# Performance work log

Hardware: AMD Instinct MI355X
Metric: run time of the kernel (lower is better)

## Reference

```python
import jax, jax.numpy as jnp
import numpy as np

N_NODES = 50000
N_EDGES = 640000
D_IN = 128
D_OUT = 128


def setup_inputs() -> dict:
    key = jax.random.key(0)
    k1, k2, k3, k4 = jax.random.split(key, 4)
    x = jax.random.normal(k1, (N_NODES, D_IN), dtype=jnp.float32)
    edge_index = jax.random.randint(k2, (2, N_EDGES), 0, N_NODES, dtype=jnp.int64)
    weight = jax.random.uniform(k3, (1,), dtype=jnp.float32)
    temperature = jnp.ones((1,), dtype=jnp.float32)
    W = jax.random.normal(k4, (D_IN, D_OUT), dtype=jnp.float32) * (1.0 / np.sqrt(D_IN))
    b = jnp.zeros((D_OUT,), dtype=jnp.float32)
    return {"x": x, "edge_index": edge_index, "weight": weight,
            "temperature": temperature, "W": W, "b": b}


def _gcn_conv(x, edge_index, W, b):
    N = x.shape[0]
    src, dst = edge_index[0], edge_index[1]
    loop = jnp.arange(N, dtype=edge_index.dtype)
    s = jnp.concatenate([src, loop])  # self-loops appended
    d = jnp.concatenate([dst, loop])
    deg = jax.ops.segment_sum(jnp.ones(s.shape[0], dtype=x.dtype), d, num_segments=N)
    dinv = jnp.where(deg > 0, deg ** -0.5, 0.0)
    norm = dinv[s] * dinv[d]  # [E+N]
    h = x @ W                 # linear transform first (PyG GCNConv)
    msg = h[s] * norm[:, None]
    out = jax.ops.segment_sum(msg, d, num_segments=N)
    return out + b


def _gradient_entropy(x, edge_index, temperature):
    # Boltzmann distribution over per-node Dirichlet energies;
    # entropy gradient w.r.t. node features (computed with autodiff).
    N = x.shape[0]
    src, dst = edge_index[0], edge_index[1]

    def entropy(z):
        diff = z[src] - z[dst]                                  # [E, D]
        E = jax.ops.segment_sum(jnp.sum(diff * diff, axis=-1), dst, num_segments=N)
        logp = jax.nn.log_softmax(-E / temperature[0])
        p = jnp.exp(logp)
        return -jnp.sum(p * logp)

    return jax.grad(entropy)(x)


def reference(x, edge_index, weight, temperature, W, b):
    h = _gcn_conv(x, edge_index, W, b)
    g = jax.lax.stop_gradient(_gradient_entropy(h, edge_index, temperature))
    return h + weight * g
```

## Files before the change

kernel.cpp:

```cpp
#include <hip/hip_runtime.h>

#define N_NODES 50000
#define N_EDGES 640000
#define NSCANB  196
#define MAXD    64
#define NBUCK   196
#define BUCKCAP 4096
#define EPB     2048
#define NPARTB  313

#define OFF_HTMPB    0
#define OFF_OBF      3200000
#define OFF_DEG      6400000
#define OFF_DINV     6450000
#define OFF_E        6500000
#define OFF_PMIN     6550000
#define OFF_PS0      6550256
#define OFF_PS1      6550512
#define OFF_WT       6550768
#define OFF_GCUR     6558960
#define OFF_PART     6559216
#define OFF_EBIN     7362032

typedef __attribute__((ext_vector_type(8))) short bf16x8;
typedef __attribute__((ext_vector_type(4))) float f32x4;

__device__ __forceinline__ unsigned short f2bf(float f) {
    unsigned u = __float_as_uint(f);
    unsigned r = u + 0x7fffu + ((u >> 16) & 1u);
    return (unsigned short)(r >> 16);
}
__device__ __forceinline__ float bflo(unsigned u) { return __uint_as_float(u << 16); }
__device__ __forceinline__ float bfhi(unsigned u) { return __uint_as_float(u & 0xffff0000u); }

__global__ __launch_bounds__(256) void k_init(const float* __restrict__ W,
                                              int* __restrict__ gcursor,
                                              unsigned short* __restrict__ wtg) {
    int gtid = blockIdx.x * 256 + threadIdx.x;
    if (gtid < NBUCK) gcursor[gtid] = 0;
    if (gtid < 4096) {
        int k = gtid >> 5, n4 = (gtid & 31) * 4;
        float4 v = *(const float4*)(W + k * 128 + n4);
        wtg[(n4 + 0) * 128 + k] = f2bf(v.x);
        wtg[(n4 + 1) * 128 + k] = f2bf(v.y);
        wtg[(n4 + 2) * 128 + k] = f2bf(v.z);
        wtg[(n4 + 3) * 128 + k] = f2bf(v.w);
    }
}

__global__ __launch_bounds__(256) void k_part(const int* __restrict__ src,
                                              const int* __restrict__ dst,
                                              int* __restrict__ gcursor,
                                              unsigned* __restrict__ part) {
    __shared__ int hist[NBUCK];
    __shared__ int base[NBUCK];
    int tid = threadIdx.x;
    if (tid < NBUCK) hist[tid] = 0;
    __syncthreads();
    int e0 = blockIdx.x * EPB;
    unsigned val[8]; int bk[8]; int rk[8];
    #pragma unroll
    for (int j = 0; j < 8; j++) {
        int e = e0 + j * 256 + tid;
        if (e < N_EDGES) {
            int s = src[e], d = dst[e];
            int bc = d >> 8;
            if ((unsigned)bc >= NBUCK) bc = NBUCK - 1;
            bk[j] = bc;
            val[j] = ((unsigned)(d & 255) << 16) | ((unsigned)s & 0xffffu);
            rk[j] = atomicAdd(&hist[bc], 1);
        } else { bk[j] = -1; val[j] = 0u; rk[j] = 0; }
    }
    __syncthreads();
    if (tid < NBUCK) base[tid] = atomicAdd(&gcursor[tid], hist[tid]);
    __syncthreads();
    #pragma unroll
    for (int j = 0; j < 8; j++) {
        if (bk[j] >= 0) {
            int p = base[bk[j]] + rk[j];
            if ((unsigned)p < BUCKCAP) part[bk[j] * BUCKCAP + p] = val[j];
        }
    }
}

__global__ __launch_bounds__(256) void k_bin(const int* __restrict__ gcursor,
                                             const unsigned* __restrict__ part,
                                             unsigned short* __restrict__ ebin,
                                             int* __restrict__ deg,
                                             float* __restrict__ dinv) {
    __shared__ __align__(16) unsigned short bins[256][MAXD];
    __shared__ int cnt[256];
    int tid = threadIdx.x, bkt = blockIdx.x;
    cnt[tid] = 0;
    __syncthreads();
    int M = gcursor[bkt];
    if (M > BUCKCAP) M = BUCKCAP;
    if (M < 0) M = 0;
    for (int i = tid; i < M; i += 256) {
        unsigned v = part[bkt * BUCKCAP + i];
        int ln = (v >> 16) & 255;
        int pos = atomicAdd(&cnt[ln], 1);
        if (pos < MAXD) bins[ln][pos] = (unsigned short)(v & 0xffffu);
    }
    __syncthreads();
    int node = bkt * 256 + tid;
    if (node < N_NODES) {
        int dg = cnt[tid]; if (dg > MAXD) dg = MAXD;
        deg[node] = dg;
        dinv[node] = rsqrtf((float)(dg + 1));
    }
    int nvalid = N_NODES - bkt * 256; if (nvalid > 256) nvalid = 256;
    if (nvalid < 0) nvalid = 0;
    int lim = nvalid * MAXD / 8;
    const uint4* bs = (const uint4*)&bins[0][0];
    uint4* gb = (uint4*)(ebin + (size_t)bkt * 256 * MAXD);
    for (int i = tid; i < lim; i += 256) gb[i] = bs[i];
}

__global__ __launch_bounds__(256) void k_gemm(const float* __restrict__ x,
                                              const unsigned short* __restrict__ wtg,
                                              const float* __restrict__ dinv,
                                              unsigned short* __restrict__ htmpb) {
    int tid = threadIdx.x;
    int wave = tid >> 6, lane = tid & 63, quad = lane >> 4, m16 = lane & 15;
    int r0 = blockIdx.x * 32 + (wave & 1) * 16;
    int ch = (wave >> 1) * 4;
    int arow = r0 + m16;
    int rowc = arow < N_NODES ? arow : N_NODES - 1;
    f32x4 acc[4];
    #pragma unroll
    for (int c = 0; c < 4; c++) acc[c] = (f32x4){0.f, 0.f, 0.f, 0.f};
    #pragma unroll
    for (int kt = 0; kt < 4; kt++) {
        int koff = kt * 32 + quad * 8;
        float4 xa = *(const float4*)(x + rowc * 128 + koff);
        float4 xb = *(const float4*)(x + rowc * 128 + koff + 4);
        bf16x8 af;
        af[0] = (short)f2bf(xa.x); af[1] = (short)f2bf(xa.y);
        af[2] = (short)f2bf(xa.z); af[3] = (short)f2bf(xa.w);
        af[4] = (short)f2bf(xb.x); af[5] = (short)f2bf(xb.y);
        af[6] = (short)f2bf(xb.z); af[7] = (short)f2bf(xb.w);
        #pragma unroll
        for (int c = 0; c < 4; c++) {
            bf16x8 bfrag = *(const bf16x8*)(wtg + ((ch + c) * 16 + m16) * 128 + koff);
            acc[c] = __builtin_amdgcn_mfma_f32_16x16x32_bf16(af, bfrag, acc[c], 0, 0, 0);
        }
    }
    #pragma unroll
    for (int reg = 0; reg < 4; reg++) {
        int grow = r0 + quad * 4 + reg;
        if (grow < N_NODES) {
            float dv = dinv[grow];
            #pragma unroll
            for (int c = 0; c < 4; c++)
                htmpb[grow * 128 + (ch + c) * 16 + m16] = f2bf(acc[c][reg] * dv);
        }
    }
}

__global__ __launch_bounds__(256) void k_gather(const unsigned short* __restrict__ htmpb,
                                                const int* __restrict__ deg,
                                                const float* __restrict__ dinv,
                                                const float* __restrict__ b,
                                                const unsigned short* __restrict__ ebin,
                                                float* __restrict__ out,
                                                unsigned short* __restrict__ obf) {
    int node = blockIdx.x * 16 + (threadIdx.x >> 4);
    int lane = threadIdx.x & 15;
    int c8 = lane * 8;
    int dg = deg[node]; if (dg > MAXD) dg = MAXD; if (dg < 0) dg = 0;
    float di = dinv[node];
    float4 bv0 = *(const float4*)(b + c8);
    float4 bv1 = *(const float4*)(b + c8 + 4);
    uint4 hv = *(const uint4*)(htmpb + node * 128 + c8);
    float a0 = bflo(hv.x), a1 = bfhi(hv.x), a2 = bflo(hv.y), a3 = bfhi(hv.y);
    float a4 = bflo(hv.z), a5 = bfhi(hv.z), a6 = bflo(hv.w), a7 = bfhi(hv.w);
    float c0 = 0.f, c1 = 0.f, c2c = 0.f, c3 = 0.f, c4 = 0.f, c5 = 0.f, c6 = 0.f, c7 = 0.f;
    const unsigned short* bin = ebin + node * MAXD;
    int k = 0;
    for (; k + 3 < dg; k += 4) {
        uint2 bw = *(const uint2*)(bin + k);
        int s0 = bw.x & 0xffff, s1 = bw.x >> 16;
        int s2 = bw.y & 0xffff, s3 = bw.y >> 16;
        uint4 u0 = *(const uint4*)(htmpb + s0 * 128 + c8);
        uint4 u1 = *(const uint4*)(htmpb + s1 * 128 + c8);
        uint4 u2 = *(const uint4*)(htmpb + s2 * 128 + c8);
        uint4 u3 = *(const uint4*)(htmpb + s3 * 128 + c8);
        a0 += bflo(u0.x); a1 += bfhi(u0.x); a2 += bflo(u0.y); a3 += bfhi(u0.y);
        a4 += bflo(u0.z); a5 += bfhi(u0.z); a6 += bflo(u0.w); a7 += bfhi(u0.w);
        c0 += bflo(u1.x); c1 += bfhi(u1.x); c2c += bflo(u1.y); c3 += bfhi(u1.y);
        c4 += bflo(u1.z); c5 += bfhi(u1.z); c6 += bflo(u1.w); c7 += bfhi(u1.w);
        a0 += bflo(u2.x); a1 += bfhi(u2.x); a2 += bflo(u2.y); a3 += bfhi(u2.y);
        a4 += bflo(u2.z); a5 += bfhi(u2.z); a6 += bflo(u2.w); a7 += bfhi(u2.w);
        c0 += bflo(u3.x); c1 += bfhi(u3.x); c2c += bflo(u3.y); c3 += bfhi(u3.y);
        c4 += bflo(u3.z); c5 += bfhi(u3.z); c6 += bflo(u3.w); c7 += bfhi(u3.w);
    }
    for (; k < dg; k++) {
        int s0 = bin[k];
        uint4 u0 = *(const uint4*)(htmpb + s0 * 128 + c8);
        a0 += bflo(u0.x); a1 += bfhi(u0.x); a2 += bflo(u0.y); a3 += bfhi(u0.y);
        a4 += bflo(u0.z); a5 += bfhi(u0.z); a6 += bflo(u0.w); a7 += bfhi(u0.w);
    }
    a0 += c0; a1 += c1; a2 += c2c; a3 += c3; a4 += c4; a5 += c5; a6 += c6; a7 += c7;
    a0 = bv0.x + di * a0; a1 = bv0.y + di * a1; a2 = bv0.z + di * a2; a3 = bv0.w + di * a3;
    a4 = bv1.x + di * a4; a5 = bv1.y + di * a5; a6 = bv1.z + di * a6; a7 = bv1.w + di * a7;
    *(float4*)(out + node * 128 + c8)     = make_float4(a0, a1, a2, a3);
    *(float4*)(out + node * 128 + c8 + 4) = make_float4(a4, a5, a6, a7);
    uint4 pk;
    pk.x = (unsigned)f2bf(a0) | ((unsigned)f2bf(a1) << 16);
    pk.y = (unsigned)f2bf(a2) | ((unsigned)f2bf(a3) << 16);
    pk.z = (unsigned)f2bf(a4) | ((unsigned)f2bf(a5) << 16);
    pk.w = (unsigned)f2bf(a6) | ((unsigned)f2bf(a7) << 16);
    *(uint4*)(obf + node * 128 + c8) = pk;
}

__global__ __launch_bounds__(256) void k_energy(const unsigned short* __restrict__ obf,
                                                const int* __restrict__ deg,
                                                const unsigned short* __restrict__ ebin,
                                                float* __restrict__ E) {
    int node = blockIdx.x * 16 + (threadIdx.x >> 4);
    int lane = threadIdx.x & 15;
    int c8 = lane * 8;
    int dg = deg[node]; if (dg > MAXD) dg = MAXD; if (dg < 0) dg = 0;
    uint4 ud = *(const uint4*)(obf + node * 128 + c8);
    float o0 = bflo(ud.x), o1 = bfhi(ud.x), o2 = bflo(ud.y), o3 = bfhi(ud.y);
    float o4 = bflo(ud.z), o5 = bfhi(ud.z), o6 = bflo(ud.w), o7 = bfhi(ud.w);
    float acc = 0.f, acc2 = 0.f;
    const unsigned short* bin = ebin + node * MAXD;
    int k = 0;
    for (; k + 3 < dg; k += 4) {
        uint2 bw = *(const uint2*)(bin + k);
        int s0 = bw.x & 0xffff, s1 = bw.x >> 16;
        int s2 = bw.y & 0xffff, s3 = bw.y >> 16;
        uint4 a = *(const uint4*)(obf + s0 * 128 + c8);
        uint4 c = *(const uint4*)(obf + s1 * 128 + c8);
        uint4 g = *(const uint4*)(obf + s2 * 128 + c8);
        uint4 h = *(const uint4*)(obf + s3 * 128 + c8);
        float d0, d1, d2, d3, d4, d5, d6, d7;
        d0 = bflo(a.x) - o0; d1 = bfhi(a.x) - o1; d2 = bflo(a.y) - o2; d3 = bfhi(a.y) - o3;
        d4 = bflo(a.z) - o4; d5 = bfhi(a.z) - o5; d6 = bflo(a.w) - o6; d7 = bfhi(a.w) - o7;
        acc  += d0*d0 + d1*d1 + d2*d2 + d3*d3 + d4*d4 + d5*d5 + d6*d6 + d7*d7;
        d0 = bflo(c.x) - o0; d1 = bfhi(c.x) - o1; d2 = bflo(c.y) - o2; d3 = bfhi(c.y) - o3;
        d4 = bflo(c.z) - o4; d5 = bfhi(c.z) - o5; d6 = bflo(c.w) - o6; d7 = bfhi(c.w) - o7;
        acc2 += d0*d0 + d1*d1 + d2*d2 + d3*d3 + d4*d4 + d5*d5 + d6*d6 + d7*d7;
        d0 = bflo(g.x) - o0; d1 = bfhi(g.x) - o1; d2 = bflo(g.y) - o2; d3 = bfhi(g.y) - o3;
        d4 = bflo(g.z) - o4; d5 = bfhi(g.z) - o5; d6 = bflo(g.w) - o6; d7 = bfhi(g.w) - o7;
        acc  += d0*d0 + d1*d1 + d2*d2 + d3*d3 + d4*d4 + d5*d5 + d6*d6 + d7*d7;
        d0 = bflo(h.x) - o0; d1 = bfhi(h.x) - o1; d2 = bflo(h.y) - o2; d3 = bfhi(h.y) - o3;
        d4 = bflo(h.z) - o4; d5 = bfhi(h.z) - o5; d6 = bflo(h.w) - o6; d7 = bfhi(h.w) - o7;
        acc2 += d0*d0 + d1*d1 + d2*d2 + d3*d3 + d4*d4 + d5*d5 + d6*d6 + d7*d7;
    }
    for (; k < dg; k++) {
        int s0 = bin[k];
        uint4 a = *(const uint4*)(obf + s0 * 128 + c8);
        float d0 = bflo(a.x) - o0, d1 = bfhi(a.x) - o1, d2 = bflo(a.y) - o2, d3 = bfhi(a.y) - o3;
        float d4 = bflo(a.z) - o4, d5 = bfhi(a.z) - o5, d6 = bflo(a.w) - o6, d7 = bfhi(a.w) - o7;
        acc += d0*d0 + d1*d1 + d2*d2 + d3*d3 + d4*d4 + d5*d5 + d6*d6 + d7*d7;
    }
    acc += acc2;
    #pragma unroll
    for (int off = 8; off; off >>= 1) acc += __shfl_xor(acc, off);
    if (lane == 0) E[node] = acc;
}

__global__ __launch_bounds__(256) void k_esoft(const float* __restrict__ E,
                                               const float* __restrict__ temp,
                                               float* __restrict__ pmin,
                                               float* __restrict__ ps0,
                                               float* __restrict__ ps1) {
    __shared__ float fred[12];
    int tid = threadIdx.x;
    int i = blockIdx.x * 256 + tid;
    int lane = tid & 63, wid = tid >> 6;
    float e = (i < N_NODES) ? E[i] : 3.402823466e38f;
    float m = e;
    #pragma unroll
    for (int off = 32; off; off >>= 1) m = fminf(m, __shfl_xor(m, off));
    if (lane == 0) fred[wid] = m;
    __syncthreads();
    float bm = fminf(fminf(fred[0], fred[1]), fminf(fred[2], fred[3]));
    float T = temp[0];
    float s0 = 0.f, s1 = 0.f;
    if (i < N_NODES) {
        float dd = (bm - e) / T;
        float ed = __expf(dd);
        s0 = ed; s1 = ed * dd;
    }
    #pragma unroll
    for (int off = 32; off; off >>= 1) { s0 += __shfl_xor(s0, off); s1 += __shfl_xor(s1, off); }
    __syncthreads();
    if (lane == 0) { fred[4 + wid] = s0; fred[8 + wid] = s1; }
    __syncthreads();
    if (tid == 0) {
        pmin[blockIdx.x] = bm;
        ps0[blockIdx.x] = fred[4] + fred[5] + fred[6] + fred[7];
        ps1[blockIdx.x] = fred[8] + fred[9] + fred[10] + fred[11];
    }
}

__global__ __launch_bounds__(256) void k_grad(const int* __restrict__ deg,
                                              const unsigned short* __restrict__ ebin,
                                              const float* __restrict__ E,
                                              const float* __restrict__ temp,
                                              const float* __restrict__ pmin,
                                              const float* __restrict__ ps0,
                                              const float* __restrict__ ps1,
                                              const float* __restrict__ weight,
                                              float* __restrict__ out) {
    __shared__ float fred[12];
    int tid = threadIdx.x;
    int lane = tid & 63, wid = tid >> 6;

    float pm = (tid < NSCANB) ? pmin[tid] : 3.402823466e38f;
    float m = pm;
    #pragma unroll
    for (int off = 32; off; off >>= 1) m = fminf(m, __shfl_xor(m, off));
    if (lane == 0) fred[wid] = m;
    __syncthreads();
    float gmin = fminf(fminf(fred[0], fred[1]), fminf(fred[2], fred[3]));
    float T = temp[0];
    float s0 = 0.f, s1 = 0.f;
    if (tid < NSCANB) {
        float dl = (gmin - pm) / T;
        float ex = __expf(dl);
        float b0 = ps0[tid], b1 = ps1[tid];
        s0 = ex * b0;
        s1 = ex * (b1 + dl * b0);
    }
    #pragma unroll
    for (int off = 32; off; off >>= 1) { s0 += __shfl_xor(s0, off); s1 += __shfl_xor(s1, off); }
    __syncthreads();
    if (lane == 0) { fred[4 + wid] = s0; fred[8 + wid] = s1; }
    __syncthreads();
    float S0 = fred[4] + fred[5] + fred[6] + fred[7];
    float S1 = fred[8] + fred[9] + fred[10] + fred[11];

    float wscale = 2.f * weight[0];
    int lane32 = tid & 31;
    int node = blockIdx.x * 8 + (tid >> 5);
    if (node >= N_NODES) return;
    float dd = (gmin - E[node]) / T;
    float qd = (__expf(dd) / S0) * (dd - S1 / S0) / T;
    if (qd == 0.f) return;
    float cc = wscale * qd;
    int dg = deg[node]; if (dg > MAXD) dg = MAXD; if (dg < 0) dg = 0;
    float4 od = *(const float4*)(out + node * 128 + lane32 * 4);
    float sx = 0.f, sy = 0.f, sz = 0.f, sw = 0.f;
    const unsigned short* bin = ebin + node * MAXD;
    for (int k = 0; k < dg; k++) {
        int s = bin[k];
        if (s >= N_NODES) s = N_NODES - 1;
        float4 a = *(const float4*)(out + s * 128 + lane32 * 4);
        float vx = cc * (a.x - od.x), vy = cc * (a.y - od.y);
        float vz = cc * (a.z - od.z), vw = cc * (a.w - od.w);
        float* os = out + s * 128 + lane32 * 4;
        atomicAdd(os + 0, vx); atomicAdd(os + 1, vy);
        atomicAdd(os + 2, vz); atomicAdd(os + 3, vw);
        sx += vx; sy += vy; sz += vz; sw += vw;
    }
    float* odp = out + node * 128 + lane32 * 4;
    atomicAdd(odp + 0, -sx); atomicAdd(odp + 1, -sy);
    atomicAdd(odp + 2, -sz); atomicAdd(odp + 3, -sw);
}

extern "C" void kernel_launch(void* const* d_in, const int* in_sizes, int n_in,
                              void* d_out, int out_size, void* d_ws, size_t ws_size,
                              hipStream_t stream) {
    const float* x      = (const float*)d_in[0];
    const int*   ei     = (const int*)d_in[1];
    const float* weight = (const float*)d_in[2];
    const float* temp   = (const float*)d_in[3];
    const float* W      = (const float*)d_in[4];
    const float* b      = (const float*)d_in[5];
    float* out = (float*)d_out;
    float* ws  = (float*)d_ws;

    const int* src = ei;
    const int* dst = ei + N_EDGES;

    unsigned short* htmpb = (unsigned short*)(ws + OFF_HTMPB);
    unsigned short* obf   = (unsigned short*)(ws + OFF_OBF);
    int*   deg      = (int*)(ws + OFF_DEG);
    float* dinv     = ws + OFF_DINV;
    float* Earr     = ws + OFF_E;
    float* pminA    = ws + OFF_PMIN;
    float* ps0A     = ws + OFF_PS0;
    float* ps1A     = ws + OFF_PS1;
    unsigned short* wtg = (unsigned short*)(ws + OFF_WT);
    int*   gcursor  = (int*)(ws + OFF_GCUR);
    unsigned* part  = (unsigned*)(ws + OFF_PART);
    unsigned short* ebin = (unsigned short*)(ws + OFF_EBIN);

    k_init<<<16, 256, 0, stream>>>(W, gcursor, wtg);
    k_part<<<NPARTB, 256, 0, stream>>>(src, dst, gcursor, part);
    k_bin<<<NBUCK, 256, 0, stream>>>(gcursor, part, ebin, deg, dinv);
    k_gemm<<<1563, 256, 0, stream>>>(x, wtg, dinv, htmpb);
    k_gather<<<3125, 256, 0, stream>>>(htmpb, deg, dinv, b, ebin, out, obf);
    k_energy<<<3125, 256, 0, stream>>>(obf, deg, ebin, Earr);
    k_esoft<<<NSCANB, 256, 0, stream>>>(Earr, temp, pminA, ps0A, ps1A);
    k_grad<<<6250, 256, 0, stream>>>(deg, ebin, Earr, temp, pminA, ps0A, ps1A, weight, out);
}
```

Measured before the change: 215.6 us.

## Process nodes in degree-sorted order in gather and energy kernels

Builds a per-degree histogram in k_bin and adds a k_order kernel that counting-sorts node ids by in-degree. The gather and energy kernels then take their node from this order array, so the 16-lane groups in a wave handle nodes of similar degree. This is meant to cut divergence and load imbalance from the variable-length neighbour loops. The cost is an extra kernel launch, global atomics, an extra indirection per node, and writes to out/obf that are no longer contiguous across groups.

```diff
diff --git a/kernel.cpp b/kernel.cpp
--- a/kernel.cpp
+++ b/kernel.cpp
@@ -21,6 +21,9 @@
 #define OFF_GCUR     6558960
 #define OFF_PART     6559216
 #define OFF_EBIN     7362032
+#define OFF_DHIST    8962032
+#define OFF_GDCUR    8962100
+#define OFF_ORDER    8962200
 
 typedef __attribute__((ext_vector_type(8))) short bf16x8;
 typedef __attribute__((ext_vector_type(4))) float f32x4;
@@ -35,9 +38,12 @@
 
 __global__ __launch_bounds__(256) void k_init(const float* __restrict__ W,
                                               int* __restrict__ gcursor,
+                                              int* __restrict__ dhist,
+                                              int* __restrict__ gdcur,
                                               unsigned short* __restrict__ wtg) {
     int gtid = blockIdx.x * 256 + threadIdx.x;
     if (gtid < NBUCK) gcursor[gtid] = 0;
+    if (gtid < 65) { dhist[gtid] = 0; gdcur[gtid] = 0; }
     if (gtid < 4096) {
         int k = gtid >> 5, n4 = (gtid & 31) * 4;
         float4 v = *(const float4*)(W + k * 128 + n4);
@@ -87,11 +93,14 @@
                                              const unsigned* __restrict__ part,
                                              unsigned short* __restrict__ ebin,
                                              int* __restrict__ deg,
-                                             float* __restrict__ dinv) {
+                                             float* __restrict__ dinv,
+                                             int* __restrict__ dhist) {
     __shared__ __align__(16) unsigned short bins[256][MAXD];
     __shared__ int cnt[256];
+    __shared__ int dh[65];
     int tid = threadIdx.x, bkt = blockIdx.x;
     cnt[tid] = 0;
+    if (tid < 65) dh[tid] = 0;
     __syncthreads();
     int M = gcursor[bkt];
     if (M > BUCKCAP) M = BUCKCAP;
@@ -108,13 +117,49 @@
         int dg = cnt[tid]; if (dg > MAXD) dg = MAXD;
         deg[node] = dg;
         dinv[node] = rsqrtf((float)(dg + 1));
-    }
+        atomicAdd(&dh[dg], 1);
+    }
+    __syncthreads();
+    if (tid < 65 && dh[tid] > 0) atomicAdd(&dhist[tid], dh[tid]);
     int nvalid = N_NODES - bkt * 256; if (nvalid > 256) nvalid = 256;
     if (nvalid < 0) nvalid = 0;
     int lim = nvalid * MAXD / 8;
     const uint4* bs = (const uint4*)&bins[0][0];
     uint4* gb = (uint4*)(ebin + (size_t)bkt * 256 * MAXD);
     for (int i = tid; i < lim; i += 256) gb[i] = bs[i];
+}
+
+__global__ __launch_bounds__(256) void k_order(const int* __restrict__ deg,
+                                               const int* __restrict__ dhist,
+                                               int* __restrict__ gdcur,
+                                               int* __restrict__ order) {
+    __shared__ int dh[65];
+    __shared__ int resv[65];
+    __shared__ int pre[65];
+    __shared__ int hval[65];
+    int tid = threadIdx.x;
+    int node = blockIdx.x * 256 + tid;
+    if (tid < 65) { dh[tid] = 0; hval[tid] = dhist[tid]; }
+    __syncthreads();
+    int dg = 0, rk = 0;
+    bool valid = node < N_NODES;
+    if (valid) {
+        dg = deg[node];
+        if (dg < 0) dg = 0; if (dg > MAXD) dg = MAXD;
+        rk = atomicAdd(&dh[dg], 1);
+    }
+    __syncthreads();
+    if (tid < 65) resv[tid] = dh[tid] > 0 ? atomicAdd(&gdcur[tid], dh[tid]) : 0;
+    if (tid == 0) {
+        int run = 0;
+        #pragma unroll 1
+        for (int d = 0; d < 65; d++) { pre[d] = run; run += hval[d]; }
+    }
+    __syncthreads();
+    if (valid) {
+        int pos = pre[dg] + resv[dg] + rk;
+        if ((unsigned)pos < N_NODES) order[pos] = node;
+    }
 }
 
 __global__ __launch_bounds__(256) void k_gemm(const float* __restrict__ x,
@@ -163,9 +208,12 @@
                                                 const float* __restrict__ dinv,
                                                 const float* __restrict__ b,
                                                 const unsigned short* __restrict__ ebin,
+                                                const int* __restrict__ order,
                                                 float* __restrict__ out,
                                                 unsigned short* __restrict__ obf) {
-    int node = blockIdx.x * 16 + (threadIdx.x >> 4);
+    int idx = blockIdx.x * 16 + (threadIdx.x >> 4);
+    int node = order[idx];
+    if ((unsigned)node >= N_NODES) node = 0;
     int lane = threadIdx.x & 15;
     int c8 = lane * 8;
     int dg = deg[node]; if (dg > MAXD) dg = MAXD; if (dg < 0) dg = 0;
@@ -217,8 +265,11 @@
 __global__ __launch_bounds__(256) void k_energy(const unsigned short* __restrict__ obf,
                                                 const int* __restrict__ deg,
                                                 const unsigned short* __restrict__ ebin,
+                                                const int* __restrict__ order,
                                                 float* __restrict__ E) {
-    int node = blockIdx.x * 16 + (threadIdx.x >> 4);
+    int idx = blockIdx.x * 16 + (threadIdx.x >> 4);
+    int node = order[idx];
+    if ((unsigned)node >= N_NODES) node = 0;
     int lane = threadIdx.x & 15;
     int c8 = lane * 8;
     int dg = deg[node]; if (dg > MAXD) dg = MAXD; if (dg < 0) dg = 0;
@@ -390,13 +441,17 @@
     int*   gcursor  = (int*)(ws + OFF_GCUR);
     unsigned* part  = (unsigned*)(ws + OFF_PART);
     unsigned short* ebin = (unsigned short*)(ws + OFF_EBIN);
-
-    k_init<<<16, 256, 0, stream>>>(W, gcursor, wtg);
+    int*   dhist    = (int*)(ws + OFF_DHIST);
+    int*   gdcur    = (int*)(ws + OFF_GDCUR);
+    int*   order    = (int*)(ws + OFF_ORDER);
+
+    k_init<<<16, 256, 0, stream>>>(W, gcursor, dhist, gdcur, wtg);
     k_part<<<NPARTB, 256, 0, stream>>>(src, dst, gcursor, part);
-    k_bin<<<NBUCK, 256, 0, stream>>>(gcursor, part, ebin, deg, dinv);
+    k_bin<<<NBUCK, 256, 0, stream>>>(gcursor, part, ebin, deg, dinv, dhist);
+    k_order<<<NSCANB, 256, 0, stream>>>(deg, dhist, gdcur, order);
     k_gemm<<<1563, 256, 0, stream>>>(x, wtg, dinv, htmpb);
-    k_gather<<<3125, 256, 0, stream>>>(htmpb, deg, dinv, b, ebin, out, obf);
-    k_energy<<<3125, 256, 0, stream>>>(obf, deg, ebin, Earr);
+    k_gather<<<3125, 256, 0, stream>>>(htmpb, deg, dinv, b, ebin, order, out, obf);
+    k_energy<<<3125, 256, 0, stream>>>(obf, deg, ebin, order, Earr);
     k_esoft<<<NSCANB, 256, 0, stream>>>(Earr, temp, pminA, ps0A, ps1A);
     k_grad<<<6250, 256, 0, stream>>>(deg, ebin, Earr, temp, pminA, ps0A, ps1A, weight, out);
 }
```

New measurement: 223.2 us. +3.5%, slower.
